# Kernel tuning notes

Hardware: AMD Instinct MI355X
Metric: run time of the kernel (lower is better)

## Reference

```python
import jax, jax.numpy as jnp
import numpy as np

N = 100000  # nodes
E = 1600000  # edges


def _gcn_norm(edge_index, num_nodes):
    # PyG GCNConv default: add self-loops, symmetric normalization.
    src, dst = edge_index[0], edge_index[1]
    loop = jnp.arange(num_nodes, dtype=src.dtype)
    src = jnp.concatenate([src, loop])
    dst = jnp.concatenate([dst, loop])
    deg = jax.ops.segment_sum(jnp.ones_like(dst, dtype=jnp.float32), dst,
                              num_segments=num_nodes)
    dinv = jnp.where(deg > 0, jax.lax.rsqrt(deg), 0.0)
    norm = dinv[src] * dinv[dst]  # [E + N]
    return src, dst, norm


def _gcn_layer(x, W, b, src, dst, norm, num_nodes):
    h = x @ W                                # [N, out]
    msg = h[src] * norm[:, None]             # gather + scale, [E+N, out]
    agg = jax.ops.segment_sum(msg, dst, num_segments=num_nodes)
    return agg + b


def setup_inputs() -> dict:
    key = jax.random.key(0)
    ks = jax.random.split(key, 8)
    d_in, d_h, d_out = 128, 128, 64
    x = jax.random.normal(ks[0], (N, d_in), dtype=jnp.float32)
    edge_index = jax.random.randint(ks[1], (2, E), 0, N, dtype=jnp.int64)
    def glorot(k, fan_in, fan_out):
        s = jnp.sqrt(6.0 / (fan_in + fan_out)).astype(jnp.float32)
        return jax.random.uniform(k, (fan_in, fan_out), jnp.float32, -s, s)
    return {
        "x": x,
        "edge_index": edge_index,
        "W1": glorot(ks[2], d_in, d_h), "b1": jnp.zeros((d_h,), jnp.float32),
        "W2": glorot(ks[3], d_h, d_h), "b2": jnp.zeros((d_h,), jnp.float32),
        "W3": glorot(ks[4], d_h, d_out), "b3": jnp.zeros((d_out,), jnp.float32),
    }


def reference(x, edge_index, W1, b1, W2, b2, W3, b3):
    src, dst, norm = _gcn_norm(edge_index, N)
    h = jax.nn.relu(_gcn_layer(x, W1, b1, src, dst, norm, N))
    h = jax.nn.relu(_gcn_layer(h, W2, b2, src, dst, norm, N))
    h = jax.nn.relu(_gcn_layer(h, W3, b3, src, dst, norm, N))
    return h
```

## Files before the change

### kernel.cpp

```cpp
#include <hip/hip_runtime.h>
#include <hip/hip_bf16.h>
#include <hip/hip_fp16.h>


constexpr int N_NODES = 100000;
constexpr int E_EDGES = 1600000;
constexpr int SCAN_B = (N_NODES + 1023) / 1024;

typedef short short8 __attribute__((ext_vector_type(8)));
typedef float f32x4 __attribute__((ext_vector_type(4)));

__global__ __launch_bounds__(256) void rank_kernel(
    const int* __restrict__ dst, int* __restrict__ cnt,
    int* __restrict__ eRank) {
  int e = blockIdx.x * 256 + threadIdx.x;
  if (e < E_EDGES) eRank[e] = atomicAdd(&cnt[dst[e]], 1);
}

__global__ __launch_bounds__(256) void scan_part_kernel(
    const int* __restrict__ cnt, int* __restrict__ bsum) {
  __shared__ int red[256];
  const int t = threadIdx.x;
  int base = blockIdx.x * 1024 + t * 4;
  int4 v = make_int4(0, 0, 0, 0);
  if (base < N_NODES) v = *(const int4*)(cnt + base);
  red[t] = v.x + v.y + v.z + v.w;
  __syncthreads();
  for (int off = 128; off > 0; off >>= 1) {
    if (t < off) red[t] += red[t + off];
    __syncthreads();
  }
  if (t == 0) bsum[blockIdx.x] = red[0];
}

__global__ __launch_bounds__(128) void scan_tops_kernel(
    const int* __restrict__ bsum, int* __restrict__ boff,
    int* __restrict__ rowptr) {
  __shared__ int part[128];
  const int t = threadIdx.x;
  int v = (t < SCAN_B) ? bsum[t] : 0;
  part[t] = v;
  __syncthreads();
  for (int off = 1; off < 128; off <<= 1) {
    int add = (t >= off) ? part[t - off] : 0;
    __syncthreads();
    part[t] += add;
    __syncthreads();
  }
  if (t < SCAN_B) boff[t] = part[t] - v;
  if (t == 127) rowptr[N_NODES] = part[127];
}

__global__ __launch_bounds__(256) void scan_write_kernel(
    const int* __restrict__ cnt, const int* __restrict__ boff,
    int* __restrict__ rowptr, float* __restrict__ dinv) {
  __shared__ int part[256];
  const int t = threadIdx.x;
  int base = blockIdx.x * 1024 + t * 4;
  int4 v = make_int4(0, 0, 0, 0);
  if (base < N_NODES) v = *(const int4*)(cnt + base);
  int s = v.x + v.y + v.z + v.w;
  part[t] = s;
  __syncthreads();
  for (int off = 1; off < 256; off <<= 1) {
    int add = (t >= off) ? part[t - off] : 0;
    __syncthreads();
    part[t] += add;
    __syncthreads();
  }
  if (base < N_NODES) {
    int run = boff[blockIdx.x] + part[t] - s;
    int4 o;
    o.x = run;
    o.y = run + v.x;
    o.z = run + v.x + v.y;
    o.w = run + v.x + v.y + v.z;
    *(int4*)(rowptr + base) = o;
    float4 dv;
    dv.x = rsqrtf((float)v.x + 1.0f);
    dv.y = rsqrtf((float)v.y + 1.0f);
    dv.z = rsqrtf((float)v.z + 1.0f);
    dv.w = rsqrtf((float)v.w + 1.0f);
    *(float4*)(dinv + base) = dv;
  }
}

__global__ __launch_bounds__(256) void place_kernel(
    const int* __restrict__ src, const int* __restrict__ dst,
    const int* __restrict__ eRank, const int* __restrict__ rowptr,
    const float* __restrict__ dinv, int2* __restrict__ eSW) {
  int e = blockIdx.x * 256 + threadIdx.x;
  if (e < E_EDGES) {
    int d = dst[e];
    int s = src[e];
    int pos = rowptr[d] + eRank[e];
    eSW[pos] = make_int2(s, __float_as_int(dinv[s] * dinv[d]));
  }
}

__device__ inline ushort bf_round(float x) {
  uint u = __float_as_uint(x);
  return (ushort)((u + 0x7FFFu + ((u >> 16) & 1u)) >> 16);
}
__device__ inline ushort bf_split(float x, float* rem) {
  ushort h = bf_round(x);
  *rem = x - __uint_as_float((uint)h << 16);
  return h;
}

template <int OC>
__global__ __launch_bounds__(256) void packw_kernel(
    const float* __restrict__ W, ushort* __restrict__ hi,
    ushort* __restrict__ lo) {
  int id = blockIdx.x * 256 + threadIdx.x;
  if (id >= OC * 16) return;
  int col = id & 15;
  int g = (id >> 4) & 3;
  int ks = (id >> 6) & 3;
  int nt = id >> 8;
  int k0 = ks * 32 + g * 8;
  int n = nt * 16 + col;
  ushort h8[8], l8[8];
#pragma unroll
  for (int j = 0; j < 8; ++j) {
    float rem;
    h8[j] = bf_split(W[(size_t)(k0 + j) * OC + n], &rem);
    l8[j] = bf_round(rem);
  }
  size_t base = (size_t)id * 8;
#pragma unroll
  for (int j = 0; j < 8; ++j) {
    hi[base + j] = h8[j];
    lo[base + j] = l8[j];
  }
}

template <int OC>
__global__ __launch_bounds__(256) void gemm_kernel(
    const float* __restrict__ X, const ushort* __restrict__ Whi,
    const ushort* __restrict__ Wlo, __half* __restrict__ H) {
  constexpr int NT = OC / 16;
  __shared__ ushort sWhi[OC * 128];
  __shared__ ushort sWlo[OC * 128];
  const int t = threadIdx.x;
  {
    const uint4* gh = (const uint4*)Whi;
    const uint4* gl = (const uint4*)Wlo;
    uint4* sh = (uint4*)sWhi;
    uint4* sl = (uint4*)sWlo;
    for (int i = t; i < OC * 128 / 8; i += 256) {
      sh[i] = gh[i];
      sl[i] = gl[i];
    }
  }
  const int wid = t >> 6;
  const int lane = t & 63;
  const int row = blockIdx.x * 64 + wid * 16 + (lane & 15);
  const bool ok = row < N_NODES;
  const int g = lane >> 4;

  short8 ahi[4], alo[4];
  const float* xr = X + (size_t)row * 128;
#pragma unroll
  for (int ks = 0; ks < 4; ++ks) {
    float f[8];
    if (ok) {
      float4 f0 = *(const float4*)(xr + ks * 32 + g * 8);
      float4 f1 = *(const float4*)(xr + ks * 32 + g * 8 + 4);
      f[0] = f0.x; f[1] = f0.y; f[2] = f0.z; f[3] = f0.w;
      f[4] = f1.x; f[5] = f1.y; f[6] = f1.z; f[7] = f1.w;
    } else {
#pragma unroll
      for (int j = 0; j < 8; ++j) f[j] = 0.f;
    }
    union { short8 v; ushort u[8]; } h, l;
#pragma unroll
    for (int j = 0; j < 8; ++j) {
      float rem;
      h.u[j] = bf_split(f[j], &rem);
      l.u[j] = bf_round(rem);
    }
    ahi[ks] = h.v;
    alo[ks] = l.v;
  }
  __syncthreads();

#pragma unroll
  for (int nt = 0; nt < NT; ++nt) {
    f32x4 acc = {0.f, 0.f, 0.f, 0.f};
#pragma unroll
    for (int ks = 0; ks < 4; ++ks) {
      int off = (((nt * 4 + ks) * 4 + g) * 16 + (lane & 15)) * 8;
      short8 bhi = *(const short8*)&sWhi[off];
      short8 blo = *(const short8*)&sWlo[off];
      acc = __builtin_amdgcn_mfma_f32_16x16x32_bf16(alo[ks], bhi, acc, 0, 0, 0);
      acc = __builtin_amdgcn_mfma_f32_16x16x32_bf16(ahi[ks], blo, acc, 0, 0, 0);
      acc = __builtin_amdgcn_mfma_f32_16x16x32_bf16(ahi[ks], bhi, acc, 0, 0, 0);
    }
#pragma unroll
    for (int r = 0; r < 4; ++r) {
      int rr = blockIdx.x * 64 + wid * 16 + g * 4 + r;
      if (rr < N_NODES)
        H[(size_t)rr * OC + nt * 16 + (lane & 15)] = __float2half(acc[r]);
    }
  }
}

template <int OC>
__global__ __launch_bounds__(256) void agg_kernel(
    const __half* __restrict__ H, const int* __restrict__ rowptr,
    const int2* __restrict__ eSW, const float* __restrict__ dinv,
    const float* __restrict__ bias, float* __restrict__ Y) {
  const int wave = threadIdx.x >> 6;
  const int lane = threadIdx.x & 63;
  const int n = blockIdx.x * 4 + wave;
  if (n >= N_NODES) return;
  const float dn = dinv[n];
  const float selfw = dn * dn;
  const int beg = rowptr[n], end = rowptr[n + 1];
  const int jal = min(beg + (beg & 1), end);
  const int jend = jal + ((end - jal) & ~7);
  const int jend2 = jend + ((end - jend) & ~1);

  if constexpr (OC == 128) {
    const __half2* H2 = (const __half2*)H;
    float2 hv = __half22float2(H2[(size_t)n * 64 + lane]);
    float ax = hv.x * selfw, ay = hv.y * selfw;
    for (int j = beg; j < jal; ++j) {
      int2 p = eSW[j];
      float2 v = __half22float2(H2[(size_t)p.x * 64 + lane]);
      float w = __int_as_float(p.y);
      ax = fmaf(v.x, w, ax);
      ay = fmaf(v.y, w, ay);
    }
    for (int j = jal; j < jend; j += 8) {
      int4 p0 = *(const int4*)(eSW + j);
      int4 p1 = *(const int4*)(eSW + j + 2);
      int4 p2 = *(const int4*)(eSW + j + 4);
      int4 p3 = *(const int4*)(eSW + j + 6);
      __half2 h0 = H2[(size_t)p0.x * 64 + lane];
      __half2 h1 = H2[(size_t)p0.z * 64 + lane];
      __half2 h2 = H2[(size_t)p1.x * 64 + lane];
      __half2 h3 = H2[(size_t)p1.z * 64 + lane];
      __half2 h4 = H2[(size_t)p2.x * 64 + lane];
      __half2 h5 = H2[(size_t)p2.z * 64 + lane];
      __half2 h6 = H2[(size_t)p3.x * 64 + lane];
      __half2 h7 = H2[(size_t)p3.z * 64 + lane];
      float2 v0 = __half22float2(h0);
      float2 v1 = __half22float2(h1);
      float2 v2 = __half22float2(h2);
      float2 v3 = __half22float2(h3);
      float2 v4 = __half22float2(h4);
      float2 v5 = __half22float2(h5);
      float2 v6 = __half22float2(h6);
      float2 v7 = __half22float2(h7);
      ax = fmaf(v0.x, __int_as_float(p0.y), ax);
      ay = fmaf(v0.y, __int_as_float(p0.y), ay);
      ax = fmaf(v1.x, __int_as_float(p0.w), ax);
      ay = fmaf(v1.y, __int_as_float(p0.w), ay);
      ax = fmaf(v2.x, __int_as_float(p1.y), ax);
      ay = fmaf(v2.y, __int_as_float(p1.y), ay);
      ax = fmaf(v3.x, __int_as_float(p1.w), ax);
      ay = fmaf(v3.y, __int_as_float(p1.w), ay);
      ax = fmaf(v4.x, __int_as_float(p2.y), ax);
      ay = fmaf(v4.y, __int_as_float(p2.y), ay);
      ax = fmaf(v5.x, __int_as_float(p2.w), ax);
      ay = fmaf(v5.y, __int_as_float(p2.w), ay);
      ax = fmaf(v6.x, __int_as_float(p3.y), ax);
      ay = fmaf(v6.y, __int_as_float(p3.y), ay);
      ax = fmaf(v7.x, __int_as_float(p3.w), ax);
      ay = fmaf(v7.y, __int_as_float(p3.w), ay);
    }
    for (int j = jend; j < jend2; j += 2) {
      int4 p = *(const int4*)(eSW + j);
      float2 v0 = __half22float2(H2[(size_t)p.x * 64 + lane]);
      float2 v1 = __half22float2(H2[(size_t)p.z * 64 + lane]);
      ax = fmaf(v0.x, __int_as_float(p.y), ax);
      ay = fmaf(v0.y, __int_as_float(p.y), ay);
      ax = fmaf(v1.x, __int_as_float(p.w), ax);
      ay = fmaf(v1.y, __int_as_float(p.w), ay);
    }
    for (int j = jend2; j < end; ++j) {
      int2 p = eSW[j];
      float2 v = __half22float2(H2[(size_t)p.x * 64 + lane]);
      float w = __int_as_float(p.y);
      ax = fmaf(v.x, w, ax);
      ay = fmaf(v.y, w, ay);
    }
    float2 bb = ((const float2*)bias)[lane];
    float2 o;
    o.x = fmaxf(ax + bb.x, 0.f);
    o.y = fmaxf(ay + bb.y, 0.f);
    ((float2*)Y)[(size_t)n * 64 + lane] = o;
  } else {
    float a = __half2float(H[(size_t)n * 64 + lane]) * selfw;
    for (int j = beg; j < jal; ++j) {
      int2 p = eSW[j];
      a = fmaf(__half2float(H[(size_t)p.x * 64 + lane]),
               __int_as_float(p.y), a);
    }
    for (int j = jal; j < jend; j += 8) {
      int4 p0 = *(const int4*)(eSW + j);
      int4 p1 = *(const int4*)(eSW + j + 2);
      int4 p2 = *(const int4*)(eSW + j + 4);
      int4 p3 = *(const int4*)(eSW + j + 6);
      __half h0 = H[(size_t)p0.x * 64 + lane];
      __half h1 = H[(size_t)p0.z * 64 + lane];
      __half h2 = H[(size_t)p1.x * 64 + lane];
      __half h3 = H[(size_t)p1.z * 64 + lane];
      __half h4 = H[(size_t)p2.x * 64 + lane];
      __half h5 = H[(size_t)p2.z * 64 + lane];
      __half h6 = H[(size_t)p3.x * 64 + lane];
      __half h7 = H[(size_t)p3.z * 64 + lane];
      a = fmaf(__half2float(h0), __int_as_float(p0.y), a);
      a = fmaf(__half2float(h1), __int_as_float(p0.w), a);
      a = fmaf(__half2float(h2), __int_as_float(p1.y), a);
      a = fmaf(__half2float(h3), __int_as_float(p1.w), a);
      a = fmaf(__half2float(h4), __int_as_float(p2.y), a);
      a = fmaf(__half2float(h5), __int_as_float(p2.w), a);
      a = fmaf(__half2float(h6), __int_as_float(p3.y), a);
      a = fmaf(__half2float(h7), __int_as_float(p3.w), a);
    }
    for (int j = jend; j < jend2; j += 2) {
      int4 p = *(const int4*)(eSW + j);
      a = fmaf(__half2float(H[(size_t)p.x * 64 + lane]),
               __int_as_float(p.y), a);
      a = fmaf(__half2float(H[(size_t)p.z * 64 + lane]),
               __int_as_float(p.w), a);
    }
    for (int j = jend2; j < end; ++j) {
      int2 p = eSW[j];
      a = fmaf(__half2float(H[(size_t)p.x * 64 + lane]),
               __int_as_float(p.y), a);
    }
    Y[(size_t)n * 64 + lane] = fmaxf(a + bias[lane], 0.f);
  }
}

extern "C" void kernel_launch(void* const* d_in, const int* in_sizes, int n_in,
                              void* d_out, int out_size, void* d_ws,
                              size_t ws_size, hipStream_t stream) {
  const float* x = (const float*)d_in[0];
  const int* ei = (const int*)d_in[1];
  const float* W1 = (const float*)d_in[2];
  const float* b1 = (const float*)d_in[3];
  const float* W2 = (const float*)d_in[4];
  const float* b2 = (const float*)d_in[5];
  const float* W3 = (const float*)d_in[6];
  const float* b3 = (const float*)d_in[7];
  const int* src = ei;
  const int* dst = ei + E_EDGES;

  size_t off = 0;
  auto alloc = [&](size_t bytes) -> void* {
    void* p = (char*)d_ws + off;
    off += (bytes + 255) & ~(size_t)255;
    return p;
  };
  int* cnt = (int*)alloc((size_t)N_NODES * 4);
  int* rowptr = (int*)alloc((size_t)(N_NODES + 1) * 4);
  float* dinv = (float*)alloc((size_t)N_NODES * 4);
  int* bsum = (int*)alloc((size_t)SCAN_B * 4);
  int* boff = (int*)alloc((size_t)SCAN_B * 4);
  int* eRank = (int*)alloc((size_t)E_EDGES * 4);
  int2* eSW = (int2*)alloc((size_t)E_EDGES * 8);
  __half* h = (__half*)alloc((size_t)N_NODES * 128 * 2);
  float* A = (float*)alloc((size_t)N_NODES * 128 * 4);
  ushort* wp1h = (ushort*)alloc((size_t)128 * 128 * 2);
  ushort* wp1l = (ushort*)alloc((size_t)128 * 128 * 2);
  ushort* wp2h = (ushort*)alloc((size_t)128 * 128 * 2);
  ushort* wp2l = (ushort*)alloc((size_t)128 * 128 * 2);
  ushort* wp3h = (ushort*)alloc((size_t)128 * 64 * 2);
  ushort* wp3l = (ushort*)alloc((size_t)128 * 64 * 2);

  hipMemsetAsync(cnt, 0, (size_t)N_NODES * 4, stream);

  const int EB = (E_EDGES + 255) / 256;
  rank_kernel<<<EB, 256, 0, stream>>>(dst, cnt, eRank);
  scan_part_kernel<<<SCAN_B, 256, 0, stream>>>(cnt, bsum);
  scan_tops_kernel<<<1, 128, 0, stream>>>(bsum, boff, rowptr);
  scan_write_kernel<<<SCAN_B, 256, 0, stream>>>(cnt, boff, rowptr, dinv);
  place_kernel<<<EB, 256, 0, stream>>>(src, dst, eRank, rowptr, dinv, eSW);
  packw_kernel<128><<<8, 256, 0, stream>>>(W1, wp1h, wp1l);
  packw_kernel<128><<<8, 256, 0, stream>>>(W2, wp2h, wp2l);
  packw_kernel<64><<<4, 256, 0, stream>>>(W3, wp3h, wp3l);

  const int GB = (N_NODES + 63) / 64;
  const int AB = (N_NODES + 3) / 4;

  gemm_kernel<128><<<GB, 256, 0, stream>>>(x, wp1h, wp1l, h);
  agg_kernel<128><<<AB, 256, 0, stream>>>(h, rowptr, eSW, dinv, b1, A);
  gemm_kernel<128><<<GB, 256, 0, stream>>>(A, wp2h, wp2l, h);
  agg_kernel<128><<<AB, 256, 0, stream>>>(h, rowptr, eSW, dinv, b2, A);
  gemm_kernel<64><<<GB, 256, 0, stream>>>(A, wp3h, wp3l, h);
  agg_kernel<64><<<AB, 256, 0, stream>>>(h, rowptr, eSW, dinv, b3,
                                         (float*)d_out);
}
```

Measured before the change: 380.0 us.

## Fuse rank with first GEMM, batch weight packing, store fp16 activations, nontemporal edge loads

Merges the three weight-pack launches into one kernel. Runs the edge-rank atomic pass and the first GEMM as disjoint block ranges of a single launch so they overlap. Stores intermediate activations as fp16 instead of fp32, which halves their write and read traffic between aggregation and GEMM. Edge-list loads and output stores now use nontemporal hints. This cuts launch overhead and memory traffic, at the cost of extra rounding of the hidden activations to fp16.

Result: slower. 402.9 us (+6.0%).

```diff
diff --git a/kernel.cpp b/kernel.cpp
--- a/kernel.cpp
+++ b/kernel.cpp
@@ -6,16 +6,12 @@
 constexpr int N_NODES = 100000;
 constexpr int E_EDGES = 1600000;
 constexpr int SCAN_B = (N_NODES + 1023) / 1024;
+constexpr int RANK_B = 2048;
 
 typedef short short8 __attribute__((ext_vector_type(8)));
 typedef float f32x4 __attribute__((ext_vector_type(4)));
-
-__global__ __launch_bounds__(256) void rank_kernel(
-    const int* __restrict__ dst, int* __restrict__ cnt,
-    int* __restrict__ eRank) {
-  int e = blockIdx.x * 256 + threadIdx.x;
-  if (e < E_EDGES) eRank[e] = atomicAdd(&cnt[dst[e]], 1);
-}
+typedef int iv4 __attribute__((ext_vector_type(4)));
+typedef float fv2 __attribute__((ext_vector_type(2)));
 
 __global__ __launch_bounds__(256) void scan_part_kernel(
     const int* __restrict__ cnt, int* __restrict__ bsum) {
@@ -108,11 +104,9 @@
   return h;
 }
 
-template <int OC>
-__global__ __launch_bounds__(256) void packw_kernel(
-    const float* __restrict__ W, ushort* __restrict__ hi,
-    ushort* __restrict__ lo) {
-  int id = blockIdx.x * 256 + threadIdx.x;
+__device__ inline void packw_body(int id, int OC, const float* __restrict__ W,
+                                  ushort* __restrict__ hi,
+                                  ushort* __restrict__ lo) {
   if (id >= OC * 16) return;
   int col = id & 15;
   int g = (id >> 4) & 3;
@@ -135,10 +129,23 @@
   }
 }
 
-template <int OC>
-__global__ __launch_bounds__(256) void gemm_kernel(
-    const float* __restrict__ X, const ushort* __restrict__ Whi,
-    const ushort* __restrict__ Wlo, __half* __restrict__ H) {
+__global__ __launch_bounds__(256) void packw_all_kernel(
+    const float* __restrict__ W1, ushort* __restrict__ h1,
+    ushort* __restrict__ l1, const float* __restrict__ W2,
+    ushort* __restrict__ h2, ushort* __restrict__ l2,
+    const float* __restrict__ W3, ushort* __restrict__ h3,
+    ushort* __restrict__ l3) {
+  int b = blockIdx.x;
+  if (b < 8) packw_body(b * 256 + threadIdx.x, 128, W1, h1, l1);
+  else if (b < 16) packw_body((b - 8) * 256 + threadIdx.x, 128, W2, h2, l2);
+  else packw_body((b - 16) * 256 + threadIdx.x, 64, W3, h3, l3);
+}
+
+template <int OC, bool HALF_IN>
+__device__ inline void gemm_body(int bid, const void* __restrict__ Xv,
+                                 const ushort* __restrict__ Whi,
+                                 const ushort* __restrict__ Wlo,
+                                 __half* __restrict__ H) {
   constexpr int NT = OC / 16;
   __shared__ ushort sWhi[OC * 128];
   __shared__ ushort sWlo[OC * 128];
@@ -155,20 +162,31 @@
   }
   const int wid = t >> 6;
   const int lane = t & 63;
-  const int row = blockIdx.x * 64 + wid * 16 + (lane & 15);
+  const int row = bid * 64 + wid * 16 + (lane & 15);
   const bool ok = row < N_NODES;
   const int g = lane >> 4;
 
   short8 ahi[4], alo[4];
-  const float* xr = X + (size_t)row * 128;
 #pragma unroll
   for (int ks = 0; ks < 4; ++ks) {
     float f[8];
     if (ok) {
-      float4 f0 = *(const float4*)(xr + ks * 32 + g * 8);
-      float4 f1 = *(const float4*)(xr + ks * 32 + g * 8 + 4);
-      f[0] = f0.x; f[1] = f0.y; f[2] = f0.z; f[3] = f0.w;
-      f[4] = f1.x; f[5] = f1.y; f[6] = f1.z; f[7] = f1.w;
+      if constexpr (HALF_IN) {
+        const __half* xr = (const __half*)Xv + (size_t)row * 128;
+        uint4 u = *(const uint4*)(xr + ks * 32 + g * 8);
+        float2 t0 = __half22float2(*(__half2*)&u.x);
+        float2 t1 = __half22float2(*(__half2*)&u.y);
+        float2 t2 = __half22float2(*(__half2*)&u.z);
+        float2 t3 = __half22float2(*(__half2*)&u.w);
+        f[0] = t0.x; f[1] = t0.y; f[2] = t1.x; f[3] = t1.y;
+        f[4] = t2.x; f[5] = t2.y; f[6] = t3.x; f[7] = t3.y;
+      } else {
+        const float* xr = (const float*)Xv + (size_t)row * 128;
+        float4 f0 = *(const float4*)(xr + ks * 32 + g * 8);
+        float4 f1 = *(const float4*)(xr + ks * 32 + g * 8 + 4);
+        f[0] = f0.x; f[1] = f0.y; f[2] = f0.z; f[3] = f0.w;
+        f[4] = f1.x; f[5] = f1.y; f[6] = f1.z; f[7] = f1.w;
+      }
     } else {
 #pragma unroll
       for (int j = 0; j < 8; ++j) f[j] = 0.f;
@@ -199,18 +217,39 @@
     }
 #pragma unroll
     for (int r = 0; r < 4; ++r) {
-      int rr = blockIdx.x * 64 + wid * 16 + g * 4 + r;
+      int rr = bid * 64 + wid * 16 + g * 4 + r;
       if (rr < N_NODES)
         H[(size_t)rr * OC + nt * 16 + (lane & 15)] = __float2half(acc[r]);
     }
   }
 }
 
-template <int OC>
+template <int OC, bool HALF_IN>
+__global__ __launch_bounds__(256) void gemm_kernel(
+    const void* __restrict__ Xv, const ushort* __restrict__ Whi,
+    const ushort* __restrict__ Wlo, __half* __restrict__ H) {
+  gemm_body<OC, HALF_IN>(blockIdx.x, Xv, Whi, Wlo, H);
+}
+
+__global__ __launch_bounds__(256) void gemm1_rank_kernel(
+    const float* __restrict__ X, const ushort* __restrict__ Whi,
+    const ushort* __restrict__ Wlo, __half* __restrict__ H,
+    const int* __restrict__ dst, int* __restrict__ cnt,
+    int* __restrict__ eRank) {
+  if (blockIdx.x < RANK_B) {
+    for (int e = blockIdx.x * 256 + threadIdx.x; e < E_EDGES;
+         e += RANK_B * 256)
+      eRank[e] = atomicAdd(&cnt[dst[e]], 1);
+  } else {
+    gemm_body<128, false>(blockIdx.x - RANK_B, X, Whi, Wlo, H);
+  }
+}
+
+template <int OC, bool HALF_OUT>
 __global__ __launch_bounds__(256) void agg_kernel(
     const __half* __restrict__ H, const int* __restrict__ rowptr,
     const int2* __restrict__ eSW, const float* __restrict__ dinv,
-    const float* __restrict__ bias, float* __restrict__ Y) {
+    const float* __restrict__ bias, void* __restrict__ out) {
   const int wave = threadIdx.x >> 6;
   const int lane = threadIdx.x & 63;
   const int n = blockIdx.x * 4 + wave;
@@ -221,6 +260,7 @@
   const int jal = min(beg + (beg & 1), end);
   const int jend = jal + ((end - jal) & ~7);
   const int jend2 = jend + ((end - jend) & ~1);
+  const int* eS = (const int*)eSW;
 
   if constexpr (OC == 128) {
     const __half2* H2 = (const __half2*)H;
@@ -234,10 +274,10 @@
       ay = fmaf(v.y, w, ay);
     }
     for (int j = jal; j < jend; j += 8) {
-      int4 p0 = *(const int4*)(eSW + j);
-      int4 p1 = *(const int4*)(eSW + j + 2);
-      int4 p2 = *(const int4*)(eSW + j + 4);
-      int4 p3 = *(const int4*)(eSW + j + 6);
+      iv4 p0 = __builtin_nontemporal_load((const iv4*)(eS + 2 * j));
+      iv4 p1 = __builtin_nontemporal_load((const iv4*)(eS + 2 * j + 4));
+      iv4 p2 = __builtin_nontemporal_load((const iv4*)(eS + 2 * j + 8));
+      iv4 p3 = __builtin_nontemporal_load((const iv4*)(eS + 2 * j + 12));
       __half2 h0 = H2[(size_t)p0.x * 64 + lane];
       __half2 h1 = H2[(size_t)p0.z * 64 + lane];
       __half2 h2 = H2[(size_t)p1.x * 64 + lane];
@@ -272,7 +312,7 @@
       ay = fmaf(v7.y, __int_as_float(p3.w), ay);
     }
     for (int j = jend; j < jend2; j += 2) {
-      int4 p = *(const int4*)(eSW + j);
+      iv4 p = __builtin_nontemporal_load((const iv4*)(eS + 2 * j));
       float2 v0 = __half22float2(H2[(size_t)p.x * 64 + lane]);
       float2 v1 = __half22float2(H2[(size_t)p.z * 64 + lane]);
       ax = fmaf(v0.x, __int_as_float(p.y), ax);
@@ -288,10 +328,17 @@
       ay = fmaf(v.y, w, ay);
     }
     float2 bb = ((const float2*)bias)[lane];
-    float2 o;
-    o.x = fmaxf(ax + bb.x, 0.f);
-    o.y = fmaxf(ay + bb.y, 0.f);
-    ((float2*)Y)[(size_t)n * 64 + lane] = o;
+    float ox = fmaxf(ax + bb.x, 0.f);
+    float oy = fmaxf(ay + bb.y, 0.f);
+    if constexpr (HALF_OUT) {
+      __half2 hp = __floats2half2_rn(ox, oy);
+      uint hb;
+      __builtin_memcpy(&hb, &hp, 4);
+      __builtin_nontemporal_store(hb, (uint*)out + (size_t)n * 64 + lane);
+    } else {
+      fv2 o = {ox, oy};
+      __builtin_nontemporal_store(o, (fv2*)out + (size_t)n * 64 + lane);
+    }
   } else {
     float a = __half2float(H[(size_t)n * 64 + lane]) * selfw;
     for (int j = beg; j < jal; ++j) {
@@ -300,10 +347,10 @@
                __int_as_float(p.y), a);
     }
     for (int j = jal; j < jend; j += 8) {
-      int4 p0 = *(const int4*)(eSW + j);
-      int4 p1 = *(const int4*)(eSW + j + 2);
-      int4 p2 = *(const int4*)(eSW + j + 4);
-      int4 p3 = *(const int4*)(eSW + j + 6);
+      iv4 p0 = __builtin_nontemporal_load((const iv4*)(eS + 2 * j));
+      iv4 p1 = __builtin_nontemporal_load((const iv4*)(eS + 2 * j + 4));
+      iv4 p2 = __builtin_nontemporal_load((const iv4*)(eS + 2 * j + 8));
+      iv4 p3 = __builtin_nontemporal_load((const iv4*)(eS + 2 * j + 12));
       __half h0 = H[(size_t)p0.x * 64 + lane];
       __half h1 = H[(size_t)p0.z * 64 + lane];
       __half h2 = H[(size_t)p1.x * 64 + lane];
@@ -322,7 +369,7 @@
       a = fmaf(__half2float(h7), __int_as_float(p3.w), a);
     }
     for (int j = jend; j < jend2; j += 2) {
-      int4 p = *(const int4*)(eSW + j);
+      iv4 p = __builtin_nontemporal_load((const iv4*)(eS + 2 * j));
       a = fmaf(__half2float(H[(size_t)p.x * 64 + lane]),
                __int_as_float(p.y), a);
       a = fmaf(__half2float(H[(size_t)p.z * 64 + lane]),
@@ -333,7 +380,8 @@
       a = fmaf(__half2float(H[(size_t)p.x * 64 + lane]),
                __int_as_float(p.y), a);
     }
-    Y[(size_t)n * 64 + lane] = fmaxf(a + bias[lane], 0.f);
+    float o = fmaxf(a + bias[lane], 0.f);
+    __builtin_nontemporal_store(o, (float*)out + (size_t)n * 64 + lane);
   }
 }
 
@@ -365,7 +413,7 @@
   int* eRank = (int*)alloc((size_t)E_EDGES * 4);
   int2* eSW = (int2*)alloc((size_t)E_EDGES * 8);
   __half* h = (__half*)alloc((size_t)N_NODES * 128 * 2);
-  float* A = (float*)alloc((size_t)N_NODES * 128 * 4);
+  __half* A = (__half*)alloc((size_t)N_NODES * 128 * 2);
   ushort* wp1h = (ushort*)alloc((size_t)128 * 128 * 2);
   ushort* wp1l = (ushort*)alloc((size_t)128 * 128 * 2);
   ushort* wp2h = (ushort*)alloc((size_t)128 * 128 * 2);
@@ -376,23 +424,22 @@
   hipMemsetAsync(cnt, 0, (size_t)N_NODES * 4, stream);
 
   const int EB = (E_EDGES + 255) / 256;
-  rank_kernel<<<EB, 256, 0, stream>>>(dst, cnt, eRank);
+  const int GB = (N_NODES + 63) / 64;
+  const int AB = (N_NODES + 3) / 4;
+
+  packw_all_kernel<<<20, 256, 0, stream>>>(W1, wp1h, wp1l, W2, wp2h, wp2l, W3,
+                                           wp3h, wp3l);
+  gemm1_rank_kernel<<<RANK_B + GB, 256, 0, stream>>>(x, wp1h, wp1l, h, dst,
+                                                     cnt, eRank);
   scan_part_kernel<<<SCAN_B, 256, 0, stream>>>(cnt, bsum);
   scan_tops_kernel<<<1, 128, 0, stream>>>(bsum, boff, rowptr);
   scan_write_kernel<<<SCAN_B, 256, 0, stream>>>(cnt, boff, rowptr, dinv);
   place_kernel<<<EB, 256, 0, stream>>>(src, dst, eRank, rowptr, dinv, eSW);
-  packw_kernel<128><<<8, 256, 0, stream>>>(W1, wp1h, wp1l);
-  packw_kernel<128><<<8, 256, 0, stream>>>(W2, wp2h, wp2l);
-  packw_kernel<64><<<4, 256, 0, stream>>>(W3, wp3h, wp3l);
-
-  const int GB = (N_NODES + 63) / 64;
-  const int AB = (N_NODES + 3) / 4;
-
-  gemm_kernel<128><<<GB, 256, 0, stream>>>(x, wp1h, wp1l, h);
-  agg_kernel<128><<<AB, 256, 0, stream>>>(h, rowptr, eSW, dinv, b1, A);
-  gemm_kernel<128><<<GB, 256, 0, stream>>>(A, wp2h, wp2l, h);
-  agg_kernel<128><<<AB, 256, 0, stream>>>(h, rowptr, eSW, dinv, b2, A);
-  gemm_kernel<64><<<GB, 256, 0, stream>>>(A, wp3h, wp3l, h);
-  agg_kernel<64><<<AB, 256, 0, stream>>>(h, rowptr, eSW, dinv, b3,
-                                         (float*)d_out);
-}
+
+  agg_kernel<128, true><<<AB, 256, 0, stream>>>(h, rowptr, eSW, dinv, b1, A);
+  gemm_kernel<128, true><<<GB, 256, 0, stream>>>(A, wp2h, wp2l, h);
+  agg_kernel<128, true><<<AB, 256, 0, stream>>>(h, rowptr, eSW, dinv, b2, A);
+  gemm_kernel<64, true><<<GB, 256, 0, stream>>>(A, wp3h, wp3l, h);
+  agg_kernel<64, false><<<AB, 256, 0, stream>>>(h, rowptr, eSW, dinv, b3,
+                                                d_out);
+}
```
